# Kernel optimization log

Measured on AMD Instinct MI355X. Metric: run time of the kernel, lower is better.

## Reference

```python
import jax, jax.numpy as jnp
import numpy as np

N_NODES = 20000
N_EDGES = 640000
HIDDEN = 256
HEADS = 8
HEAD_DIM = HIDDEN // HEADS
VOCAB = 119
N_FEATS = 9


def setup_inputs() -> dict:
    key = jax.random.key(0)
    ks = jax.random.split(key, 12)
    X = jax.random.randint(ks[0], (N_NODES, N_FEATS), 0, VOCAB)
    edge_row = jnp.sort(jax.random.randint(ks[1], (N_EDGES,), 0, N_NODES))
    edge_col = jax.random.randint(ks[2], (N_EDGES,), 0, N_NODES)
    s = 0.05  # init scale to keep activations sane
    emb_tables = jax.random.normal(ks[3], (N_FEATS, VOCAB, HIDDEN), jnp.float32) * s
    q_w = jax.random.normal(ks[4], (HIDDEN, HIDDEN), jnp.float32) * s
    q_b = jax.random.normal(ks[5], (HIDDEN,), jnp.float32) * s
    k_w = jax.random.normal(ks[6], (HIDDEN, HIDDEN), jnp.float32) * s
    k_b = jax.random.normal(ks[7], (HIDDEN,), jnp.float32) * s
    v_w = jax.random.normal(ks[8], (HIDDEN, HIDDEN), jnp.float32) * s
    v_b = jax.random.normal(ks[9], (HIDDEN,), jnp.float32) * s
    o_w = jax.random.normal(ks[10], (HIDDEN, HIDDEN), jnp.float32) * s
    o_b = jax.random.normal(ks[11], (HIDDEN,), jnp.float32) * s
    return dict(X=X, edge_row=edge_row, edge_col=edge_col, emb_tables=emb_tables,
                q_w=q_w, q_b=q_b, k_w=k_w, k_b=k_b, v_w=v_w, v_b=v_b, o_w=o_w, o_b=o_b)


def reference(X, edge_row, edge_col, emb_tables, q_w, q_b, k_w, k_b, v_w, v_b, o_w, o_b):
    N = X.shape[0]
    # AtomEncoder: sum of per-feature embeddings -> [N, HIDDEN]
    feat_idx = jnp.arange(N_FEATS)[None, :]  # [1, 9]
    h = emb_tables[feat_idx, X].sum(axis=1)  # [N, 9, H] -> [N, H]
    # q/k/v projections (torch Linear: y = x W^T + b), split into heads
    q = (h @ q_w.T + q_b).reshape(N, HEADS, HEAD_DIM) * (HEAD_DIM ** -0.5)
    k = (h @ k_w.T + k_b).reshape(N, HEADS, HEAD_DIM)
    v = (h @ v_w.T + v_b).reshape(N, HEADS, HEAD_DIM)
    # SDDMM: per-edge, per-head scores
    s = jnp.einsum('ehd,ehd->eh', q[edge_row], k[edge_col])  # [E, HEADS]
    # sparse row-wise softmax (over each node's outgoing-edge neighbors)
    m = jax.ops.segment_max(s, edge_row, num_segments=N)
    e = jnp.exp(s - m[edge_row])
    z = jax.ops.segment_sum(e, edge_row, num_segments=N)
    attn = e / z[edge_row]  # [E, HEADS]
    # SPMM: weighted aggregation of neighbor values
    out = jax.ops.segment_sum(attn[:, :, None] * v[edge_col], edge_row, num_segments=N)
    return out.reshape(N, HIDDEN) @ o_w.T + o_b
```

## Files before the change

kernel.cpp:

```cpp
#include <hip/hip_runtime.h>
#include <hip/hip_bf16.h>

#define N_NODES 20000
#define N_EDGES 640000
#define HIDDEN 256
#define HEADS 8
#define HEAD_DIM 32
#define N_FEATS 9
#define VOCAB 119

typedef __hip_bfloat16 bf16;
typedef __attribute__((ext_vector_type(8))) short short8;
typedef __attribute__((ext_vector_type(4))) float f32x4;

__device__ __forceinline__ ushort f2u(float x) { union { ushort u; bf16 b; } c; c.b = __float2bfloat16(x); return c.u; }
__device__ __forceinline__ void unpack8(uint4 u, float* f) {
    f[0] = __uint_as_float(u.x << 16); f[1] = __uint_as_float(u.x & 0xffff0000u);
    f[2] = __uint_as_float(u.y << 16); f[3] = __uint_as_float(u.y & 0xffff0000u);
    f[4] = __uint_as_float(u.z << 16); f[5] = __uint_as_float(u.z & 0xffff0000u);
    f[6] = __uint_as_float(u.w << 16); f[7] = __uint_as_float(u.w & 0xffff0000u);
}
__device__ __forceinline__ uint pack2(float a, float b) {
    union { __hip_bfloat162 h; uint u; } c;
    c.h = __float22bfloat162_rn(make_float2(a, b));
    return c.u;
}

#if __has_builtin(__builtin_amdgcn_fdot2_f32_bf16)
typedef __attribute__((ext_vector_type(2))) __bf16 bf16x2_t;
__device__ __forceinline__ float dot2bf(uint a, uint b, float c) {
    return __builtin_amdgcn_fdot2_f32_bf16(__builtin_bit_cast(bf16x2_t, a),
                                           __builtin_bit_cast(bf16x2_t, b), c, false);
}
#else
__device__ __forceinline__ float dot2bf(uint a, uint b, float c) {
    return c + __uint_as_float(a << 16) * __uint_as_float(b << 16)
             + __uint_as_float(a & 0xffff0000u) * __uint_as_float(b & 0xffff0000u);
}
#endif

__device__ __forceinline__ void async_ld16(const void* g, void* l) {
#if __has_builtin(__builtin_amdgcn_global_load_lds)
    __builtin_amdgcn_global_load_lds(
        (const __attribute__((address_space(1))) unsigned int*)g,
        (__attribute__((address_space(3))) unsigned int*)l, 16, 0, 0);
#else
    *(short8*)l = *(const short8*)g;
#endif
}

__global__ void k_pre(const int* __restrict__ X, const float* __restrict__ emb,
                      bf16* __restrict__ h,
                      const float* __restrict__ qw, const float* __restrict__ kw,
                      const float* __restrict__ vw, const float* __restrict__ ow,
                      const float* __restrict__ qb, const float* __restrict__ kb,
                      const float* __restrict__ vb,
                      bf16* __restrict__ wqkv, bf16* __restrict__ wo,
                      float* __restrict__ qkvb,
                      const int* __restrict__ erow, int* __restrict__ row_ptr) {
    int b = blockIdx.x;
    if (b < 5000) {
        int tid = b * 256 + threadIdx.x;
        int n = tid >> 6;
        int c4 = (tid & 63) * 4;
        float4 a = make_float4(0.f, 0.f, 0.f, 0.f);
#pragma unroll
        for (int f = 0; f < N_FEATS; ++f) {
            int idx = X[n * N_FEATS + f];
            float4 e = *(const float4*)(emb + ((size_t)(f * VOCAB + idx)) * HIDDEN + c4);
            a.x += e.x; a.y += e.y; a.z += e.z; a.w += e.w;
        }
        ushort4 o = make_ushort4(f2u(a.x), f2u(a.y), f2u(a.z), f2u(a.w));
        *(ushort4*)((ushort*)h + (size_t)n * HIDDEN + c4) = o;
    } else if (b < 6027) {
        int i = (b - 5000) * 256 + threadIdx.x;
        if (i < 196608) {
            const float* s = i < 65536 ? qw : i < 131072 ? kw : vw;
            wqkv[i] = __float2bfloat16(s[i & 65535]);
        } else if (i < 262144) {
            wo[i - 196608] = __float2bfloat16(ow[i - 196608]);
        } else if (i < 262912) {
            int j = i - 262144;
            const float* s = j < 256 ? qb : j < 512 ? kb : vb;
            qkvb[j] = s[j & 255];
        }
    } else {
        int n = (b - 6027) * 256 + threadIdx.x;
        if (n > N_NODES) return;
        int lo = 0, hi = N_EDGES;
        while (lo < hi) {
            int mid = (lo + hi) >> 1;
            if (erow[mid] < n) lo = mid + 1; else hi = mid;
        }
        row_ptr[n] = lo;
    }
}

template <int MODE, bool GUARD>
__device__ __forceinline__ void gemm_core(const bf16* __restrict__ A,
                                          const bf16* __restrict__ W,
                                          const float* __restrict__ bias,
                                          void* __restrict__ Y0, void* __restrict__ Y1,
                                          float s_q, int n0, int d0) {
    __shared__ short Bs[2][128 * 64];
    int t = threadIdx.x;
    int lane = t & 63, w = t >> 6;
    int wr = (w >> 1) * 64, wc = (w & 1) * 64;
    int lr = lane & 15, quad = lane >> 4;

    f32x4 acc[4][4] = {};

    int srow[4], scc[4], sbase[4];
#pragma unroll
    for (int it = 0; it < 4; ++it) {
        int s = it * 256 + t;
        int r = s >> 3;
        srow[it]  = r;
        scc[it]   = (s & 7) ^ (r & 7);
        sbase[it] = (it * 256 + (t & ~63)) * 8;
    }

#pragma unroll
    for (int it = 0; it < 4; ++it)
        async_ld16(W + (size_t)(d0 + srow[it]) * HIDDEN + scc[it] * 8, &Bs[0][sbase[it]]);
    __syncthreads();

    int cur = 0;
#pragma unroll 1
    for (int k0 = 64; k0 < 256; k0 += 64) {
        int kbase = k0 - 64;
        short8 af[4][2], bfr[4][2];
#pragma unroll
        for (int i = 0; i < 4; ++i)
#pragma unroll
            for (int kk = 0; kk < 2; ++kk)
                af[i][kk] = *(const short8*)(A + (size_t)(n0 + wr + i * 16 + lr) * HIDDEN
                                             + kbase + kk * 32 + quad * 8);
#pragma unroll
        for (int it = 0; it < 4; ++it)
            async_ld16(W + (size_t)(d0 + srow[it]) * HIDDEN + k0 + scc[it] * 8,
                       &Bs[cur ^ 1][sbase[it]]);
#pragma unroll
        for (int j = 0; j < 4; ++j)
#pragma unroll
            for (int kk = 0; kk < 2; ++kk) {
                int rB = wc + j * 16 + lr;
                int slot = rB * 8 + ((kk * 4 + quad) ^ (lr & 7));
                bfr[j][kk] = *(short8*)(&Bs[cur][slot * 8]);
            }
#pragma unroll
        for (int kk = 0; kk < 2; ++kk)
#pragma unroll
            for (int i = 0; i < 4; ++i)
#pragma unroll
                for (int j = 0; j < 4; ++j)
                    acc[i][j] = __builtin_amdgcn_mfma_f32_16x16x32_bf16(
                        af[i][kk], bfr[j][kk], acc[i][j], 0, 0, 0);
        __syncthreads();
        cur ^= 1;
    }
    {
        short8 af[4][2], bfr[4][2];
#pragma unroll
        for (int i = 0; i < 4; ++i)
#pragma unroll
            for (int kk = 0; kk < 2; ++kk)
                af[i][kk] = *(const short8*)(A + (size_t)(n0 + wr + i * 16 + lr) * HIDDEN
                                             + 192 + kk * 32 + quad * 8);
#pragma unroll
        for (int j = 0; j < 4; ++j)
#pragma unroll
            for (int kk = 0; kk < 2; ++kk) {
                int rB = wc + j * 16 + lr;
                int slot = rB * 8 + ((kk * 4 + quad) ^ (lr & 7));
                bfr[j][kk] = *(short8*)(&Bs[cur][slot * 8]);
            }
#pragma unroll
        for (int kk = 0; kk < 2; ++kk)
#pragma unroll
            for (int i = 0; i < 4; ++i)
#pragma unroll
                for (int j = 0; j < 4; ++j)
                    acc[i][j] = __builtin_amdgcn_mfma_f32_16x16x32_bf16(
                        af[i][kk], bfr[j][kk], acc[i][j], 0, 0, 0);
    }

#pragma unroll
    for (int j = 0; j < 4; ++j) {
        int dbase = d0 + wc + j * 16;
        float bj = bias[dbase + lr];
        if constexpr (MODE == 0) {
            float sc = (dbase < 256) ? s_q : 1.f;
            ushort* dst; int stride;
            if (dbase < 256) {
                dst = (ushort*)Y0 + (size_t)(dbase >> 6) * N_NODES * 64 + (dbase & 63) + lr;
                stride = 64;
            } else if (dbase < 512) {
                int e = dbase - 256;
                dst = (ushort*)Y1 + (size_t)(e >> 6) * N_NODES * 128 + (e & 63) + lr;
                stride = 128;
            } else {
                int e = dbase - 512;
                dst = (ushort*)Y1 + (size_t)(e >> 6) * N_NODES * 128 + 64 + (e & 63) + lr;
                stride = 128;
            }
#pragma unroll
            for (int i = 0; i < 4; ++i)
#pragma unroll
                for (int r = 0; r < 4; ++r) {
                    int n = n0 + wr + i * 16 + quad * 4 + r;
                    if (GUARD && n >= N_NODES) continue;
                    dst[(size_t)n * stride] = f2u((acc[i][j][r] + bj) * sc);
                }
        } else {
            float* dst = (float*)Y0 + dbase + lr;
#pragma unroll
            for (int i = 0; i < 4; ++i)
#pragma unroll
                for (int r = 0; r < 4; ++r) {
                    int n = n0 + wr + i * 16 + quad * 4 + r;
                    if (GUARD && n >= N_NODES) continue;
                    dst[(size_t)n * HIDDEN] = acc[i][j][r] + bj;
                }
        }
    }
}

__global__ __launch_bounds__(256, 2) void k_gemm_qkv(
    const bf16* __restrict__ A, const bf16* __restrict__ wqkv,
    const float* __restrict__ qkvb, ushort* __restrict__ qhp,
    ushort* __restrict__ kvhp, float qscale) {
    int n0 = blockIdx.x * 128;
    if (n0 + 128 <= N_NODES)
        gemm_core<0, false>(A, wqkv, qkvb, qhp, kvhp, qscale, n0, blockIdx.y * 128);
    else
        gemm_core<0, true>(A, wqkv, qkvb, qhp, kvhp, qscale, n0, blockIdx.y * 128);
}

__global__ __launch_bounds__(256, 2) void k_gemm_o(
    const bf16* __restrict__ A, const bf16* __restrict__ W,
    const float* __restrict__ bias, float* __restrict__ Y) {
    int n0 = blockIdx.x * 128;
    if (n0 + 128 <= N_NODES)
        gemm_core<1, false>(A, W, bias, Y, nullptr, 1.f, n0, blockIdx.y * 128);
    else
        gemm_core<1, true>(A, W, bias, Y, nullptr, 1.f, n0, blockIdx.y * 128);
}

__global__ __launch_bounds__(256) void k_attn(
    const int* __restrict__ row_ptr, const int* __restrict__ col,
    const ushort* __restrict__ qhp, const ushort* __restrict__ kvhp,
    bf16* __restrict__ agg) {
    int b = blockIdx.x;
    int x = b & 7;
    int hp = x & 3;
    int wave = threadIdx.x >> 6;
    int n = (b >> 3) * 8 + (x >> 2) * 4 + wave;
    int lane = threadIdx.x & 63;
    int my = lane >> 3;
    int d8 = lane & 7;

    int start = row_ptr[n];
    int deg = row_ptr[n + 1] - start;

    ushort* orow = (ushort*)agg + (size_t)n * HIDDEN + hp * 64 + d8 * 8;
    if (deg == 0) {
        if (lane < 8) { uint4 zo = {}; *(uint4*)orow = zo; }
        return;
    }

    const ushort* qrow = qhp + ((size_t)hp * N_NODES + n) * 64;
    uint4 qu = *(const uint4*)(qrow + d8 * 8);

    const ushort* kvbase = kvhp + (size_t)hp * N_NODES * 128;
    const int* cb = col + start;

    int c_all = cb[min(lane, deg - 1)];

    float z = 0.f;
    float av[8] = {};

#pragma unroll 2
    for (int i = 0; i < deg; i += 8) {
        int idx = i + my;
        int cidx = idx < deg ? idx : deg - 1;
        int c = (deg <= 64) ? __shfl(c_all, cidx) : cb[cidx];

        const ushort* kp = kvbase + (((uint)c << 7) + (uint)d8 * 8);
        uint4 ku = *(const uint4*)(kp);
        uint4 vu = *(const uint4*)(kp + 64);

        float s = dot2bf(ku.x, qu.x, 0.f);
        s = dot2bf(ku.y, qu.y, s);
        s = dot2bf(ku.z, qu.z, s);
        s = dot2bf(ku.w, qu.w, s);
        s += __shfl_xor(s, 1);
        s += __shfl_xor(s, 2);

        float p = (idx < deg) ? __expf(s) : 0.f;
        z += p;

        float vf[8];
        unpack8(vu, vf);
#pragma unroll
        for (int d = 0; d < 8; ++d) av[d] += p * vf[d];
    }

    z += __shfl_xor(z, 8); z += __shfl_xor(z, 16); z += __shfl_xor(z, 32);
#pragma unroll
    for (int d = 0; d < 8; ++d) {
        av[d] += __shfl_xor(av[d], 8);
        av[d] += __shfl_xor(av[d], 16);
        av[d] += __shfl_xor(av[d], 32);
    }

    if (lane < 8) {
        float invz = 1.f / z;
        uint4 o;
        o.x = pack2(av[0] * invz, av[1] * invz);
        o.y = pack2(av[2] * invz, av[3] * invz);
        o.z = pack2(av[4] * invz, av[5] * invz);
        o.w = pack2(av[6] * invz, av[7] * invz);
        *(uint4*)orow = o;
    }
}

extern "C" void kernel_launch(void* const* d_in, const int* in_sizes, int n_in,
                              void* d_out, int out_size, void* d_ws, size_t ws_size,
                              hipStream_t stream) {
    const int*   X    = (const int*)d_in[0];
    const int*   erow = (const int*)d_in[1];
    const int*   ecol = (const int*)d_in[2];
    const float* emb  = (const float*)d_in[3];
    const float* q_w  = (const float*)d_in[4];
    const float* q_b  = (const float*)d_in[5];
    const float* k_w  = (const float*)d_in[6];
    const float* k_b  = (const float*)d_in[7];
    const float* v_w  = (const float*)d_in[8];
    const float* v_b  = (const float*)d_in[9];
    const float* o_w  = (const float*)d_in[10];
    const float* o_b  = (const float*)d_in[11];
    float* out = (float*)d_out;

    char* ws = (char*)d_ws;
    bf16*   h    = (bf16*)(ws);
    bf16*   agg  = (bf16*)(ws);
    ushort* qhp  = (ushort*)(ws + 10240000);
    ushort* kvhp = (ushort*)(ws + 20480000);
    bf16*   wqkv = (bf16*)(ws + 40960000);
    bf16*   wo   = (bf16*)(ws + 41353216);
    float*  qkvb = (float*)(ws + 41484288);
    int* row_ptr = (int*)(ws + 41487360);

    k_pre<<<6106, 256, 0, stream>>>(X, emb, h, q_w, k_w, v_w, o_w,
                                    q_b, k_b, v_b, wqkv, wo, qkvb, erow, row_ptr);

    const float qscale = 0.17677669529663687f;
    dim3 gqkv((N_NODES + 127) / 128, 768 / 128);
    k_gemm_qkv<<<gqkv, 256, 0, stream>>>(h, wqkv, qkvb, qhp, kvhp, qscale);

    k_attn<<<N_NODES, 256, 0, stream>>>(row_ptr, ecol, qhp, kvhp, agg);

    dim3 go((N_NODES + 127) / 128, HIDDEN / 128);
    k_gemm_o<<<go, 256, 0, stream>>>(agg, wo, o_b, out);
}
```

Baseline: 190.4 us.

## Stage A and B tiles through padded LDS with register prefetch; shrink O-GEMM tile

```diff
diff --git a/kernel.cpp b/kernel.cpp
--- a/kernel.cpp
+++ b/kernel.cpp
@@ -38,16 +38,6 @@
              + __uint_as_float(a & 0xffff0000u) * __uint_as_float(b & 0xffff0000u);
 }
 #endif
-
-__device__ __forceinline__ void async_ld16(const void* g, void* l) {
-#if __has_builtin(__builtin_amdgcn_global_load_lds)
-    __builtin_amdgcn_global_load_lds(
-        (const __attribute__((address_space(1))) unsigned int*)g,
-        (__attribute__((address_space(3))) unsigned int*)l, 16, 0, 0);
-#else
-    *(short8*)l = *(const short8*)g;
-#endif
-}
 
 __global__ void k_pre(const int* __restrict__ X, const float* __restrict__ emb,
                       bf16* __restrict__ h,
@@ -96,89 +86,99 @@
     }
 }
 
-template <int MODE, bool GUARD>
+template <int MODE, bool GUARD, int TM>
 __device__ __forceinline__ void gemm_core(const bf16* __restrict__ A,
                                           const bf16* __restrict__ W,
                                           const float* __restrict__ bias,
                                           void* __restrict__ Y0, void* __restrict__ Y1,
                                           float s_q, int n0, int d0) {
-    __shared__ short Bs[2][128 * 64];
+    constexpr int RI = TM / 32;
+    __shared__ short As[TM * 72];
+    __shared__ short Bs[128 * 72];
     int t = threadIdx.x;
     int lane = t & 63, w = t >> 6;
-    int wr = (w >> 1) * 64, wc = (w & 1) * 64;
+    int wr = (w >> 1) * (TM / 2), wc = (w & 1) * 64;
     int lr = lane & 15, quad = lane >> 4;
 
-    f32x4 acc[4][4] = {};
-
-    int srow[4], scc[4], sbase[4];
-#pragma unroll
-    for (int it = 0; it < 4; ++it) {
-        int s = it * 256 + t;
-        int r = s >> 3;
-        srow[it]  = r;
-        scc[it]   = (s & 7) ^ (r & 7);
-        sbase[it] = (it * 256 + (t & ~63)) * 8;
-    }
-
+    f32x4 acc[RI][4] = {};
+    short8 ra[RI], rb[4];
+    int srowA[RI], skoA[RI], srowB[4], skoB[4];
+#pragma unroll
+    for (int it = 0; it < RI; ++it) { int c = t + 256 * it; srowA[it] = c >> 3; skoA[it] = (c & 7) * 8; }
+#pragma unroll
+    for (int it = 0; it < 4; ++it) { int c = t + 256 * it; srowB[it] = c >> 3; skoB[it] = (c & 7) * 8; }
+
+#pragma unroll
+    for (int it = 0; it < RI; ++it) {
+        int n = n0 + srowA[it];
+        short8 av = {};
+        if (!GUARD || n < N_NODES) av = *(const short8*)(A + (size_t)n * HIDDEN + skoA[it]);
+        ra[it] = av;
+    }
 #pragma unroll
     for (int it = 0; it < 4; ++it)
-        async_ld16(W + (size_t)(d0 + srow[it]) * HIDDEN + scc[it] * 8, &Bs[0][sbase[it]]);
+        rb[it] = *(const short8*)(W + (size_t)(d0 + srowB[it]) * HIDDEN + skoB[it]);
+#pragma unroll
+    for (int it = 0; it < RI; ++it) *(short8*)(&As[srowA[it] * 72 + skoA[it]]) = ra[it];
+#pragma unroll
+    for (int it = 0; it < 4; ++it)  *(short8*)(&Bs[srowB[it] * 72 + skoB[it]]) = rb[it];
     __syncthreads();
 
-    int cur = 0;
-#pragma unroll 1
     for (int k0 = 64; k0 < 256; k0 += 64) {
-        int kbase = k0 - 64;
-        short8 af[4][2], bfr[4][2];
-#pragma unroll
-        for (int i = 0; i < 4; ++i)
+#pragma unroll
+        for (int it = 0; it < RI; ++it) {
+            int n = n0 + srowA[it];
+            short8 av = {};
+            if (!GUARD || n < N_NODES) av = *(const short8*)(A + (size_t)n * HIDDEN + k0 + skoA[it]);
+            ra[it] = av;
+        }
+#pragma unroll
+        for (int it = 0; it < 4; ++it)
+            rb[it] = *(const short8*)(W + (size_t)(d0 + srowB[it]) * HIDDEN + k0 + skoB[it]);
+        {
+            short8 af[RI][2], bfr[4][2];
+#pragma unroll
+            for (int i = 0; i < RI; ++i)
+#pragma unroll
+                for (int kk = 0; kk < 2; ++kk)
+                    af[i][kk] = *(short8*)(&As[(wr + i * 16 + lr) * 72 + kk * 32 + quad * 8]);
+#pragma unroll
+            for (int j = 0; j < 4; ++j)
+#pragma unroll
+                for (int kk = 0; kk < 2; ++kk)
+                    bfr[j][kk] = *(short8*)(&Bs[(wc + j * 16 + lr) * 72 + kk * 32 + quad * 8]);
 #pragma unroll
             for (int kk = 0; kk < 2; ++kk)
-                af[i][kk] = *(const short8*)(A + (size_t)(n0 + wr + i * 16 + lr) * HIDDEN
-                                             + kbase + kk * 32 + quad * 8);
-#pragma unroll
-        for (int it = 0; it < 4; ++it)
-            async_ld16(W + (size_t)(d0 + srow[it]) * HIDDEN + k0 + scc[it] * 8,
-                       &Bs[cur ^ 1][sbase[it]]);
+#pragma unroll
+                for (int i = 0; i < RI; ++i)
+#pragma unroll
+                    for (int j = 0; j < 4; ++j)
+                        acc[i][j] = __builtin_amdgcn_mfma_f32_16x16x32_bf16(
+                            af[i][kk], bfr[j][kk], acc[i][j], 0, 0, 0);
+        }
+        __syncthreads();
+#pragma unroll
+        for (int it = 0; it < RI; ++it) *(short8*)(&As[srowA[it] * 72 + skoA[it]]) = ra[it];
+#pragma unroll
+        for (int it = 0; it < 4; ++it)  *(short8*)(&Bs[srowB[it] * 72 + skoB[it]]) = rb[it];
+        __syncthreads();
+    }
+    {
+        short8 af[RI][2], bfr[4][2];
+#pragma unroll
+        for (int i = 0; i < RI; ++i)
+#pragma unroll
+            for (int kk = 0; kk < 2; ++kk)
+                af[i][kk] = *(short8*)(&As[(wr + i * 16 + lr) * 72 + kk * 32 + quad * 8]);
 #pragma unroll
         for (int j = 0; j < 4; ++j)
 #pragma unroll
-            for (int kk = 0; kk < 2; ++kk) {
-                int rB = wc + j * 16 + lr;
-                int slot = rB * 8 + ((kk * 4 + quad) ^ (lr & 7));
-                bfr[j][kk] = *(short8*)(&Bs[cur][slot * 8]);
-            }
+            for (int kk = 0; kk < 2; ++kk)
+                bfr[j][kk] = *(short8*)(&Bs[(wc + j * 16 + lr) * 72 + kk * 32 + quad * 8]);
 #pragma unroll
         for (int kk = 0; kk < 2; ++kk)
 #pragma unroll
-            for (int i = 0; i < 4; ++i)
-#pragma unroll
-                for (int j = 0; j < 4; ++j)
-                    acc[i][j] = __builtin_amdgcn_mfma_f32_16x16x32_bf16(
-                        af[i][kk], bfr[j][kk], acc[i][j], 0, 0, 0);
-        __syncthreads();
-        cur ^= 1;
-    }
-    {
-        short8 af[4][2], bfr[4][2];
-#pragma unroll
-        for (int i = 0; i < 4; ++i)
-#pragma unroll
-            for (int kk = 0; kk < 2; ++kk)
-                af[i][kk] = *(const short8*)(A + (size_t)(n0 + wr + i * 16 + lr) * HIDDEN
-                                             + 192 + kk * 32 + quad * 8);
-#pragma unroll
-        for (int j = 0; j < 4; ++j)
-#pragma unroll
-            for (int kk = 0; kk < 2; ++kk) {
-                int rB = wc + j * 16 + lr;
-                int slot = rB * 8 + ((kk * 4 + quad) ^ (lr & 7));
-                bfr[j][kk] = *(short8*)(&Bs[cur][slot * 8]);
-            }
-#pragma unroll
-        for (int kk = 0; kk < 2; ++kk)
-#pragma unroll
-            for (int i = 0; i < 4; ++i)
+            for (int i = 0; i < RI; ++i)
 #pragma unroll
                 for (int j = 0; j < 4; ++j)
                     acc[i][j] = __builtin_amdgcn_mfma_f32_16x16x32_bf16(
@@ -205,7 +205,7 @@
                 stride = 128;
             }
 #pragma unroll
-            for (int i = 0; i < 4; ++i)
+            for (int i = 0; i < RI; ++i)
 #pragma unroll
                 for (int r = 0; r < 4; ++r) {
                     int n = n0 + wr + i * 16 + quad * 4 + r;
@@ -215,7 +215,7 @@
         } else {
             float* dst = (float*)Y0 + dbase + lr;
 #pragma unroll
-            for (int i = 0; i < 4; ++i)
+            for (int i = 0; i < RI; ++i)
 #pragma unroll
                 for (int r = 0; r < 4; ++r) {
                     int n = n0 + wr + i * 16 + quad * 4 + r;
@@ -232,19 +232,19 @@
     ushort* __restrict__ kvhp, float qscale) {
     int n0 = blockIdx.x * 128;
     if (n0 + 128 <= N_NODES)
-        gemm_core<0, false>(A, wqkv, qkvb, qhp, kvhp, qscale, n0, blockIdx.y * 128);
+        gemm_core<0, false, 128>(A, wqkv, qkvb, qhp, kvhp, qscale, n0, blockIdx.y * 128);
     else
-        gemm_core<0, true>(A, wqkv, qkvb, qhp, kvhp, qscale, n0, blockIdx.y * 128);
-}
-
-__global__ __launch_bounds__(256, 2) void k_gemm_o(
+        gemm_core<0, true, 128>(A, wqkv, qkvb, qhp, kvhp, qscale, n0, blockIdx.y * 128);
+}
+
+__global__ __launch_bounds__(256, 4) void k_gemm_o(
     const bf16* __restrict__ A, const bf16* __restrict__ W,
     const float* __restrict__ bias, float* __restrict__ Y) {
-    int n0 = blockIdx.x * 128;
-    if (n0 + 128 <= N_NODES)
-        gemm_core<1, false>(A, W, bias, Y, nullptr, 1.f, n0, blockIdx.y * 128);
+    int n0 = blockIdx.x * 64;
+    if (n0 + 64 <= N_NODES)
+        gemm_core<1, false, 64>(A, W, bias, Y, nullptr, 1.f, n0, blockIdx.y * 128);
     else
-        gemm_core<1, true>(A, W, bias, Y, nullptr, 1.f, n0, blockIdx.y * 128);
+        gemm_core<1, true, 64>(A, W, bias, Y, nullptr, 1.f, n0, blockIdx.y * 128);
 }
 
 __global__ __launch_bounds__(256) void k_attn(
@@ -361,6 +361,6 @@
 
     k_attn<<<N_NODES, 256, 0, stream>>>(row_ptr, ecol, qhp, kvhp, agg);
 
-    dim3 go((N_NODES + 127) / 128, HIDDEN / 128);
+    dim3 go((N_NODES + 63) / 64, HIDDEN / 128);
     k_gemm_o<<<go, 256, 0, stream>>>(agg, wo, o_b, out);
 }
```

New measurement: 180.1 us. 1.06x faster.
